# Optimization experiments

Hardware: AMD Instinct MI355X
Metric: run time of the kernel (lower is better)

The kernel has to match this reference:

```python
import jax, jax.numpy as jnp
import numpy as np

NUM_HEADS = 16
NUM_BUCKETS = 32
MAX_DISTANCE = 128


def _rel_bucket(rel):
    # bidirectional T5-style relative position bucketing
    nb = NUM_BUCKETS // 2
    ret = (rel > 0).astype(jnp.int32) * nb
    n = jnp.abs(rel)
    max_exact = nb // 2
    is_small = n < max_exact
    safe = jnp.maximum(n, 1).astype(jnp.float32)
    large = max_exact + (jnp.log(safe / max_exact) / np.log(MAX_DISTANCE / max_exact) * (nb - max_exact)).astype(jnp.int32)
    large = jnp.minimum(large, nb - 1)
    return ret + jnp.where(is_small, n, large)


def setup_inputs() -> dict:
    key = jax.random.key(0)
    ks = jax.random.split(key, 12)
    S, B, E = 1024, 4, 1024
    D = E // NUM_HEADS
    s = 0.02
    return {
        "query": jax.random.normal(ks[0], (S, B, E), jnp.float32),
        "q_w": jax.random.normal(ks[1], (E, E), jnp.float32) * s,
        "q_b": jnp.zeros((E,), jnp.float32),
        "k_w": jax.random.normal(ks[2], (E, E), jnp.float32) * s,
        "k_b": jnp.zeros((E,), jnp.float32),
        "v_w": jax.random.normal(ks[3], (E, E), jnp.float32) * s,
        "v_b": jnp.zeros((E,), jnp.float32),
        "out_w": jax.random.normal(ks[4], (E, E), jnp.float32) * s,
        "out_b": jnp.zeros((E,), jnp.float32),
        "rel_emb": jax.random.normal(ks[5], (NUM_BUCKETS, NUM_HEADS), jnp.float32) * s,
        "grep_w": jax.random.normal(ks[6], (8, D), jnp.float32) * s,
        "grep_b": jnp.zeros((8,), jnp.float32),
        "grep_a": jnp.ones((NUM_HEADS,), jnp.float32),
    }


def reference(query, q_w, q_b, k_w, k_b, v_w, v_b, out_w, out_b, rel_emb, grep_w, grep_b, grep_a):
    S, B, E = query.shape
    H = NUM_HEADS
    D = E // H
    scaling = D ** -0.5

    q = (query @ q_w.T + q_b) * scaling  # scaling applied before gating, as in WavLM
    k = query @ k_w.T + k_b
    v = query @ v_w.T + v_b

    def split(x):  # (S,B,E) -> (B,H,S,D)
        return x.reshape(S, B, H, D).transpose(1, 2, 0, 3)

    q4, k4, v4 = split(q), split(k), split(v)

    attn = jnp.einsum('bhqd,bhkd->bhqk', q4, k4)  # (B,H,S,S)

    pos = jnp.arange(S)
    bucket = _rel_bucket(pos[None, :] - pos[:, None])  # (S,S)
    pbias = rel_emb[bucket].transpose(2, 0, 1)          # (H,S,S)

    # GRU-gated relative position scaling
    g = jnp.einsum('bhsd,ed->bhse', q4, grep_w) + grep_b      # (B,H,S,8)
    g = jax.nn.sigmoid(g.reshape(B, H, S, 2, 4).sum(-1))     # (B,H,S,2)
    gate_a, gate_b = g[..., 0], g[..., 1]
    gate = gate_a * (gate_b * grep_a[None, :, None] - 1.0) + 2.0  # (B,H,S)

    attn = attn + gate[..., None] * pbias[None]
    probs = jax.nn.softmax(attn, axis=-1)
    ctx = jnp.einsum('bhqk,bhkd->bhqd', probs, v4)  # (B,H,S,D)
    out = ctx.transpose(2, 0, 1, 3).reshape(S, B, E) @ out_w.T + out_b
    return out
```

## Files before the change

### kernel.cpp

```cpp
#include <hip/hip_runtime.h>
#include <stdint.h>


typedef short bf16x8 __attribute__((ext_vector_type(8)));
typedef float f32x4 __attribute__((ext_vector_type(4)));

#define MFMA_BF16(a, b, c) __builtin_amdgcn_mfma_f32_16x16x32_bf16((a), (b), (c), 0, 0, 0)

#define LOG2E 1.44269504088896f
#define LN2 0.693147180559945f

__device__ __forceinline__ unsigned short f2bf(float x) {
  union { float f; unsigned u; } v; v.f = x;
  unsigned r = v.u + 0x7fffu + ((v.u >> 16) & 1u);
  return (unsigned short)(r >> 16);
}
__device__ __forceinline__ float bf2f(unsigned short u) {
  union { unsigned u; float f; } v; v.u = ((unsigned)u) << 16;
  return v.f;
}

__device__ __forceinline__ void gload_lds16(const void* g, void* l) {
  __builtin_amdgcn_global_load_lds(
      (const __attribute__((address_space(1))) unsigned int*)g,
      (__attribute__((address_space(3))) unsigned int*)l, 16, 0, 0);
}

__device__ __forceinline__ int swz(int row) { return (row ^ (row >> 2)) & 3; }

__global__ __launch_bounds__(256) void prep_kernel(
    const float* __restrict__ query, const float* __restrict__ q_w,
    const float* __restrict__ k_w, const float* __restrict__ v_w,
    const float* __restrict__ out_w, unsigned short* __restrict__ q_bf,
    unsigned short* __restrict__ wq, unsigned short* __restrict__ wk,
    unsigned short* __restrict__ wv, unsigned short* __restrict__ ohi,
    unsigned short* __restrict__ olo) {
  int i = blockIdx.x * 256 + threadIdx.x;
  if (i < 4194304) {
    int e = i & 1023;
    int sb = i >> 10;
    int s = sb >> 2, b = sb & 3;
    q_bf[((size_t)(b * 1024 + s) << 10) | e] = f2bf(query[i]);
  } else {
    int j = i - 4194304;
    wq[j] = f2bf(q_w[j]);
    wk[j] = f2bf(k_w[j]);
    wv[j] = f2bf(v_w[j]);
    float x = out_w[j];
    unsigned short h = f2bf(x);
    ohi[j] = h;
    olo[j] = f2bf(x - bf2f(h));
  }
}

__global__ __launch_bounds__(256) void relbias_kernel(const float* __restrict__ rel_emb,
                                                      float* __restrict__ bias_d) {
  int idx = blockIdx.x * 256 + threadIdx.x;
  if (idx >= 2048) return;
  if (idx == 2047) {
#pragma unroll
    for (int h = 0; h < 16; ++h) bias_d[h * 2048 + idx] = 0.f;
    return;
  }
  int rel = idx - 1023;
  int n = rel < 0 ? -rel : rel;
  int ret = rel > 0 ? 16 : 0;
  int bucket;
  if (n < 8) {
    bucket = ret + n;
  } else {
    int large = 8 + (int)(logf((float)n / 8.0f) / logf(16.0f) * 8.0f);
    if (large > 15) large = 15;
    bucket = ret + large;
  }
#pragma unroll
  for (int h = 0; h < 16; ++h)
    bias_d[h * 2048 + idx] = rel_emb[bucket * 16 + h] * LOG2E;
}

__global__ __launch_bounds__(256, 2) void qkv_gemm_kernel(
    const unsigned short* __restrict__ A, const unsigned short* __restrict__ Wq,
    const unsigned short* __restrict__ Wk, const unsigned short* __restrict__ Wv,
    const float* __restrict__ qb, const float* __restrict__ kb, const float* __restrict__ vb,
    unsigned short* __restrict__ qh,
    unsigned short* __restrict__ kh,
    unsigned short* __restrict__ vT)
{
  __shared__ __align__(16) unsigned short As[128 * 32];
  __shared__ __align__(16) unsigned short Bs[128 * 32];
  const int tid = threadIdx.x, lane = tid & 63;
  const int wv_ = tid >> 6;
  const int nt = blockIdx.x;
  const int mt = blockIdx.y;
  const int mat = nt >> 3;
  const unsigned short* W = mat == 0 ? Wq : (mat == 1 ? Wk : Wv);
  const int n0 = (nt & 7) * 128;
  const int m0 = mt * 128;
  const int moff = (wv_ & 1) * 64;
  const int noff = (wv_ >> 1) * 64;

  f32x4 acc[4][4] = {};
  const char* Ab = (const char*)A;
  const char* Wb = (const char*)W;

  int st_row[2], st_g[2];
#pragma unroll
  for (int c = 0; c < 2; ++c) {
    int o = c * 4096 + tid * 16;
    int row = o >> 6, p = (o >> 4) & 3;
    st_row[c] = row;
    st_g[c] = p ^ swz(row);
  }

  for (int kt = 0; kt < 32; ++kt) {
    __syncthreads();
#pragma unroll
    for (int c = 0; c < 2; ++c) {
      int o = c * 4096 + tid * 16;
      size_t ga = (size_t)(m0 + st_row[c]) * 2048 + (size_t)kt * 64 + st_g[c] * 16;
      size_t gb = (size_t)(n0 + st_row[c]) * 2048 + (size_t)kt * 64 + st_g[c] * 16;
      gload_lds16(Ab + ga, (char*)As + o);
      gload_lds16(Wb + gb, (char*)Bs + o);
    }
    __syncthreads();

    bf16x8 af[4], bfr[4];
#pragma unroll
    for (int i = 0; i < 4; ++i) {
      int ra = moff + i * 16 + (lane & 15);
      int rb = noff + i * 16 + (lane & 15);
      int q = lane >> 4;
      af[i] = *(const bf16x8*)((const char*)As + ra * 64 + (q ^ swz(ra)) * 16);
      bfr[i] = *(const bf16x8*)((const char*)Bs + rb * 64 + (q ^ swz(rb)) * 16);
    }
#pragma unroll
    for (int i = 0; i < 4; ++i)
#pragma unroll
      for (int j = 0; j < 4; ++j) acc[i][j] = MFMA_BF16(af[i], bfr[j], acc[i][j]);
  }

  const int bidx = m0 >> 10;
  const int s00 = (m0 & 1023) + moff + ((lane >> 4) << 2);
  const int c0 = n0 + noff + (lane & 15);
  if (mat < 2) {
    const float* barr = mat == 0 ? qb : kb;
    unsigned short* dst = mat == 0 ? qh : kh;
    const float scale = mat == 0 ? (0.125f * LOG2E) : 1.0f;
#pragma unroll
    for (int j = 0; j < 4; ++j) {
      int col = c0 + j * 16;
      int hh = col >> 6, dd = col & 63;
      float bias = barr[col];
#pragma unroll
      for (int i = 0; i < 4; ++i)
#pragma unroll
        for (int r = 0; r < 4; ++r) {
          int s = s00 + i * 16 + r;
          dst[((size_t)(bidx * 16 + hh) * 1024 + s) * 64 + dd] =
              f2bf((acc[i][j][r] + bias) * scale);
        }
    }
  } else {
#pragma unroll
    for (int j = 0; j < 4; ++j) {
      int col = c0 + j * 16;
      int hh = col >> 6, dd = col & 63;
      float bias = vb[col];
#pragma unroll
      for (int i = 0; i < 4; ++i) {
        int s = s00 + i * 16;
        ushort4 pk;
        pk.x = f2bf(acc[i][j][0] + bias);
        pk.y = f2bf(acc[i][j][1] + bias);
        pk.z = f2bf(acc[i][j][2] + bias);
        pk.w = f2bf(acc[i][j][3] + bias);
        *(ushort4*)&vT[((size_t)(bidx * 16 + hh) * 64 + dd) * 1024 + s] = pk;
      }
    }
  }
}

__global__ __launch_bounds__(256) void gate_kernel(const unsigned short* __restrict__ qh,
                                                   const float* __restrict__ grep_w,
                                                   const float* __restrict__ grep_b,
                                                   const float* __restrict__ grep_a,
                                                   float* __restrict__ gate) {
  __shared__ float gw[512];
  __shared__ float gbb[8];
  __shared__ float gaa[16];
  int tid = threadIdx.x;
  for (int i = tid; i < 512; i += 256) gw[i] = grep_w[i];
  if (tid < 8) gbb[tid] = grep_b[tid];
  if (tid < 16) gaa[tid] = grep_a[tid];
  __syncthreads();
  int idx = blockIdx.x * 256 + tid;
  int h = (idx >> 10) & 15;
  const unsigned short* qrow = qh + (size_t)idx * 64;
  float a[8] = {0.f, 0.f, 0.f, 0.f, 0.f, 0.f, 0.f, 0.f};
#pragma unroll
  for (int c = 0; c < 8; ++c) {
    bf16x8 v = *(const bf16x8*)(qrow + c * 8);
#pragma unroll
    for (int jj = 0; jj < 8; ++jj) {
      float qv = bf2f((unsigned short)v[jj]);
      int d = c * 8 + jj;
#pragma unroll
      for (int e = 0; e < 8; ++e) a[e] += qv * gw[e * 64 + d];
    }
  }
  float sa = (a[0] + a[1] + a[2] + a[3]) * LN2 + gbb[0] + gbb[1] + gbb[2] + gbb[3];
  float sb = (a[4] + a[5] + a[6] + a[7]) * LN2 + gbb[4] + gbb[5] + gbb[6] + gbb[7];
  float siga = 1.f / (1.f + __expf(-sa));
  float sigb = 1.f / (1.f + __expf(-sb));
  gate[idx] = siga * (sigb * gaa[h] - 1.f) + 2.f;
}

__global__ __launch_bounds__(512, 4) void attn_kernel(
    const unsigned short* __restrict__ qh, const unsigned short* __restrict__ kh,
    const unsigned short* __restrict__ vT, const float* __restrict__ gate,
    const float* __restrict__ bias_d, unsigned short* __restrict__ ctx_hi,
    unsigned short* __restrict__ ctx_lo) {
  __shared__ __align__(16) char smem[59392];
  const int tid = threadIdx.x, lane = tid & 63, w = tid >> 6;
  const int bh = blockIdx.x;
  const int h = bh & 15;
  const int s0 = blockIdx.y * 128;
  const int sqb = s0 + w * 16;
  const int q15 = lane & 15, quad = lane >> 4;

  float* biasrow = (float*)(smem + 51200);
  unsigned short* pw = (unsigned short*)(smem + 32768) + w * 1152 + q15 * 72;

  ((float4*)biasrow)[tid] = ((const float4*)(bias_d + h * 2048))[tid];

  const char* kbase = (const char*)(kh + (size_t)bh * 65536);
  const char* vbase = (const char*)(vT + (size_t)bh * 65536);

  const int o = tid * 16;
  const int srow = o >> 7;
  const int sg = ((o >> 4) & 7) ^ (srow & 7);
  const size_t koff = (size_t)srow * 128 + sg * 16;
  const size_t voff = (size_t)srow * 2048 + sg * 16;

  gload_lds16(kbase + koff, smem + o);
  gload_lds16(vbase + voff, smem + 16384 + o);

  const unsigned short* qbase = qh + ((size_t)bh * 1024 + sqb + q15) * 64 + (quad << 3);
  bf16x8 qf0 = *(const bf16x8*)(qbase);
  bf16x8 qf1 = *(const bf16x8*)(qbase + 32);

  const int sq = sqb + q15;
  const float gate_lane = gate[bh * 1024 + sq];

  float l_run = 0.f;
  f32x4 acc_o[4] = {};

  for (int kc = 0; kc < 16; ++kc) {
    __syncthreads();
    const char* Kc = smem + (kc & 1) * 8192;
    const char* Vc = smem + 16384 + (kc & 1) * 8192;
    if (kc < 15) {
      int nb = (kc + 1) & 1;
      gload_lds16(kbase + (size_t)(kc + 1) * 8192 + koff, smem + nb * 8192 + o);
      gload_lds16(vbase + (size_t)(kc + 1) * 128 + voff, smem + 16384 + nb * 8192 + o);
    }

    f32x4 sacc[4] = {};
#pragma unroll
    for (int t = 0; t < 4; ++t) {
      int key = t * 16 + q15;
#pragma unroll
      for (int dc = 0; dc < 2; ++dc) {
        int c16 = dc * 4 + quad;
        bf16x8 ak = *(const bf16x8*)(Kc + key * 128 + ((c16 ^ (key & 7)) << 4));
        sacc[t] = MFMA_BF16(ak, dc ? qf1 : qf0, sacc[t]);
      }
    }

    const int boff = kc * 64 - sq + 1023 + (quad << 2);
    float p[16];
    float ps = 0.f;
#pragma unroll
    for (int t = 0; t < 4; ++t)
#pragma unroll
      for (int r = 0; r < 4; ++r) {
        float v = __builtin_fmaf(gate_lane, biasrow[boff + t * 16 + r], sacc[t][r]);
        float e = __builtin_exp2f(v);
        p[t * 4 + r] = e;
        ps += e;
      }
    l_run += ps;

#pragma unroll
    for (int t = 0; t < 4; ++t) {
      ushort4 pk;
      pk.x = f2bf(p[t * 4 + 0]);
      pk.y = f2bf(p[t * 4 + 1]);
      pk.z = f2bf(p[t * 4 + 2]);
      pk.w = f2bf(p[t * 4 + 3]);
      *(ushort4*)(pw + t * 16 + (quad << 2)) = pk;
    }

#pragma unroll
    for (int ch = 0; ch < 2; ++ch) {
      bf16x8 pb = *(const bf16x8*)(pw + ch * 32 + (quad << 3));
#pragma unroll
      for (int t = 0; t < 4; ++t) {
        int d = t * 16 + q15;
        int c16 = ch * 4 + quad;
        bf16x8 av = *(const bf16x8*)(Vc + d * 128 + ((c16 ^ (d & 7)) << 4));
        acc_o[t] = MFMA_BF16(av, pb, acc_o[t]);
      }
    }
  }

  l_run += __shfl_xor(l_run, 16, 64);
  l_run += __shfl_xor(l_run, 32, 64);
  const float inv = 1.0f / l_run;

  __syncthreads();
  float* Ot = (float*)smem;
  {
    float* ow = Ot + (w * 16 + q15) * 65;
#pragma unroll
    for (int t = 0; t < 4; ++t)
#pragma unroll
      for (int r = 0; r < 4; ++r) ow[t * 16 + (quad << 2) + r] = acc_o[t][r] * inv;
  }
  __syncthreads();
  {
    int row = tid >> 2, dg = tid & 3;
    int s = s0 + row;
    const float* src = Ot + row * 65 + dg * 16;
    unsigned short hibuf[16], lobuf[16];
#pragma unroll
    for (int j = 0; j < 16; ++j) {
      float v = src[j];
      unsigned short hu = f2bf(v);
      hibuf[j] = hu;
      lobuf[j] = f2bf(v - bf2f(hu));
    }
    size_t base = (size_t)(s * 4 + (bh >> 4)) * 1024 + h * 64 + dg * 16;
#pragma unroll
    for (int half = 0; half < 2; ++half) {
      *(uint4*)(ctx_hi + base + half * 8) = *(const uint4*)(hibuf + half * 8);
      *(uint4*)(ctx_lo + base + half * 8) = *(const uint4*)(lobuf + half * 8);
    }
  }
}

__global__ __launch_bounds__(256, 3) void outproj_kernel(
    const unsigned short* __restrict__ Ahi, const unsigned short* __restrict__ Alo,
    const unsigned short* __restrict__ Bhi, const unsigned short* __restrict__ Blo,
    const float* __restrict__ ob, float* __restrict__ out) {
  __shared__ __align__(16) char smem[49152];
  const int tid = threadIdx.x, lane = tid & 63, wv_ = tid >> 6;
  const int q15 = lane & 15, quad = lane >> 4;
  const int n0 = blockIdx.x * 128;
  const int m0 = blockIdx.y * 64;
  const int moff = (wv_ & 1) * 32;
  const int noff = (wv_ >> 1) * 64;

  const int oa = tid * 16;
  const int ra_ = oa >> 6;
  const int ga_ = (((oa >> 4) & 3) ^ swz(ra_)) << 4;
  int rb_[2], gb_[2], obo_[2];
#pragma unroll
  for (int c = 0; c < 2; ++c) {
    int ob2 = c * 4096 + tid * 16;
    obo_[c] = ob2;
    rb_[c] = ob2 >> 6;
    gb_[c] = (((ob2 >> 4) & 3) ^ swz(rb_[c])) << 4;
  }

#define OP_STAGE(kt, buf)                                                        \
  {                                                                              \
    char* bb = smem + (buf)*24576;                                               \
    size_t ga = (size_t)(m0 + ra_) * 2048 + (size_t)(kt)*64 + ga_;               \
    gload_lds16((const char*)Ahi + ga, bb + oa);                                 \
    gload_lds16((const char*)Alo + ga, bb + 4096 + oa);                          \
    _Pragma("unroll") for (int c = 0; c < 2; ++c) {                              \
      size_t gb = (size_t)(n0 + rb_[c]) * 2048 + (size_t)(kt)*64 + gb_[c];       \
      gload_lds16((const char*)Bhi + gb, bb + 8192 + obo_[c]);                   \
      gload_lds16((const char*)Blo + gb, bb + 16384 + obo_[c]);                  \
    }                                                                            \
  }

  f32x4 acc[2][4] = {};
  OP_STAGE(0, 0);
  for (int kt = 0; kt < 32; ++kt) {
    __syncthreads();
    const char* base = smem + (kt & 1) * 24576;
    if (kt < 31) OP_STAGE(kt + 1, (kt + 1) & 1);

    bf16x8 ah[2], al[2], bhf[4], blf[4];
#pragma unroll
    for (int i = 0; i < 2; ++i) {
      int ra = moff + i * 16 + q15;
      int pa = (quad ^ swz(ra)) << 4;
      ah[i] = *(const bf16x8*)(base + ra * 64 + pa);
      al[i] = *(const bf16x8*)(base + 4096 + ra * 64 + pa);
    }
#pragma unroll
    for (int j = 0; j < 4; ++j) {
      int rb = noff + j * 16 + q15;
      int pb = (quad ^ swz(rb)) << 4;
      bhf[j] = *(const bf16x8*)(base + 8192 + rb * 64 + pb);
      blf[j] = *(const bf16x8*)(base + 16384 + rb * 64 + pb);
    }
#pragma unroll
    for (int i = 0; i < 2; ++i)
#pragma unroll
      for (int j = 0; j < 4; ++j) {
        f32x4 t = MFMA_BF16(al[i], bhf[j], acc[i][j]);
        t = MFMA_BF16(ah[i], blf[j], t);
        acc[i][j] = MFMA_BF16(ah[i], bhf[j], t);
      }
  }
#undef OP_STAGE

  const int rr0 = m0 + moff + (quad << 2);
  const int c0 = n0 + noff + q15;
#pragma unroll
  for (int j = 0; j < 4; ++j) {
    int col = c0 + j * 16;
    float bias = ob[col];
#pragma unroll
    for (int i = 0; i < 2; ++i)
#pragma unroll
      for (int r = 0; r < 4; ++r)
        out[(size_t)(rr0 + i * 16 + r) * 1024 + col] = acc[i][j][r] + bias;
  }
}

extern "C" void kernel_launch(void* const* d_in, const int* in_sizes, int n_in,
                              void* d_out, int out_size, void* d_ws, size_t ws_size,
                              hipStream_t stream) {
  const float* query = (const float*)d_in[0];
  const float* q_w = (const float*)d_in[1];
  const float* q_b = (const float*)d_in[2];
  const float* k_w = (const float*)d_in[3];
  const float* k_b = (const float*)d_in[4];
  const float* v_w = (const float*)d_in[5];
  const float* v_b = (const float*)d_in[6];
  const float* out_w = (const float*)d_in[7];
  const float* out_b = (const float*)d_in[8];
  const float* rel_emb = (const float*)d_in[9];
  const float* grep_w = (const float*)d_in[10];
  const float* grep_b = (const float*)d_in[11];
  const float* grep_a = (const float*)d_in[12];
  float* out = (float*)d_out;

  const size_t MB = 1u << 20;
  char* ws = (char*)d_ws;
  unsigned short* q_bf = (unsigned short*)(ws);
  unsigned short* wq_bf = (unsigned short*)(ws + 8 * MB);
  unsigned short* wk_bf = (unsigned short*)(ws + 10 * MB);
  unsigned short* wv_bf = (unsigned short*)(ws + 12 * MB);
  unsigned short* ow_hi = (unsigned short*)(ws + 14 * MB);
  unsigned short* ow_lo = (unsigned short*)(ws + 16 * MB);
  unsigned short* qhp = (unsigned short*)(ws + 18 * MB);
  unsigned short* khp = (unsigned short*)(ws + 26 * MB);
  unsigned short* vTp = (unsigned short*)(ws + 34 * MB);
  unsigned short* ctxh = (unsigned short*)(ws + 42 * MB);
  unsigned short* ctxl = (unsigned short*)(ws + 50 * MB);
  float* gatep = (float*)(ws + 58 * MB);
  float* biasp = (float*)(ws + 58 * MB + 256 * 1024);

  prep_kernel<<<20480, 256, 0, stream>>>(query, q_w, k_w, v_w, out_w, q_bf, wq_bf, wk_bf,
                                         wv_bf, ow_hi, ow_lo);
  relbias_kernel<<<8, 256, 0, stream>>>(rel_emb, biasp);
  qkv_gemm_kernel<<<dim3(24, 32), 256, 0, stream>>>(q_bf, wq_bf, wk_bf, wv_bf, q_b, k_b, v_b,
                                                    qhp, khp, vTp);
  gate_kernel<<<256, 256, 0, stream>>>(qhp, grep_w, grep_b, grep_a, gatep);
  attn_kernel<<<dim3(64, 8), 512, 0, stream>>>(qhp, khp, vTp, gatep, biasp, ctxh, ctxl);
  outproj_kernel<<<dim3(8, 64), 256, 0, stream>>>(ctxh, ctxl, ow_hi, ow_lo, out_b, out);
}
```

Measured before the change: 218.6 us.

## Double-buffer QKV GEMM, merge relbias into prep, shrink attention LDS

Folds the relative-bias table kernel into the prep kernel, removing one launch. Double-buffers the QKV GEMM's shared-memory tiles so the next K-slice load overlaps the MFMAs, dropping one barrier per iteration, and raises its occupancy hint. In attention, only the needed bias window is loaded, the per-warp P scratch is made compact with an XOR swizzle, and exp/pack is fused per tile, cutting LDS so more blocks fit per CU. The GEMM now uses 32KB of LDS per block, and the higher occupancy hints may cost registers or cause spills.

```diff
diff --git a/kernel.cpp b/kernel.cpp
--- a/kernel.cpp
+++ b/kernel.cpp
@@ -31,17 +31,18 @@
 __global__ __launch_bounds__(256) void prep_kernel(
     const float* __restrict__ query, const float* __restrict__ q_w,
     const float* __restrict__ k_w, const float* __restrict__ v_w,
-    const float* __restrict__ out_w, unsigned short* __restrict__ q_bf,
-    unsigned short* __restrict__ wq, unsigned short* __restrict__ wk,
-    unsigned short* __restrict__ wv, unsigned short* __restrict__ ohi,
-    unsigned short* __restrict__ olo) {
+    const float* __restrict__ out_w, const float* __restrict__ rel_emb,
+    unsigned short* __restrict__ q_bf, unsigned short* __restrict__ wq,
+    unsigned short* __restrict__ wk, unsigned short* __restrict__ wv,
+    unsigned short* __restrict__ ohi, unsigned short* __restrict__ olo,
+    float* __restrict__ bias_d) {
   int i = blockIdx.x * 256 + threadIdx.x;
   if (i < 4194304) {
     int e = i & 1023;
     int sb = i >> 10;
     int s = sb >> 2, b = sb & 3;
     q_bf[((size_t)(b * 1024 + s) << 10) | e] = f2bf(query[i]);
-  } else {
+  } else if (i < 5242880) {
     int j = i - 4194304;
     wq[j] = f2bf(q_w[j]);
     wk[j] = f2bf(k_w[j]);
@@ -50,35 +51,32 @@
     unsigned short h = f2bf(x);
     ohi[j] = h;
     olo[j] = f2bf(x - bf2f(h));
-  }
-}
-
-__global__ __launch_bounds__(256) void relbias_kernel(const float* __restrict__ rel_emb,
-                                                      float* __restrict__ bias_d) {
-  int idx = blockIdx.x * 256 + threadIdx.x;
-  if (idx >= 2048) return;
-  if (idx == 2047) {
-#pragma unroll
-    for (int h = 0; h < 16; ++h) bias_d[h * 2048 + idx] = 0.f;
-    return;
-  }
-  int rel = idx - 1023;
-  int n = rel < 0 ? -rel : rel;
-  int ret = rel > 0 ? 16 : 0;
-  int bucket;
-  if (n < 8) {
-    bucket = ret + n;
   } else {
-    int large = 8 + (int)(logf((float)n / 8.0f) / logf(16.0f) * 8.0f);
-    if (large > 15) large = 15;
-    bucket = ret + large;
-  }
-#pragma unroll
-  for (int h = 0; h < 16; ++h)
-    bias_d[h * 2048 + idx] = rel_emb[bucket * 16 + h] * LOG2E;
-}
-
-__global__ __launch_bounds__(256, 2) void qkv_gemm_kernel(
+    int idx = i - 5242880;
+    if (idx >= 2048) return;
+    if (idx == 2047) {
+#pragma unroll
+      for (int h = 0; h < 16; ++h) bias_d[h * 2048 + idx] = 0.f;
+      return;
+    }
+    int rel = idx - 1023;
+    int n = rel < 0 ? -rel : rel;
+    int ret = rel > 0 ? 16 : 0;
+    int bucket;
+    if (n < 8) {
+      bucket = ret + n;
+    } else {
+      int large = 8 + (int)(logf((float)n / 8.0f) / logf(16.0f) * 8.0f);
+      if (large > 15) large = 15;
+      bucket = ret + large;
+    }
+#pragma unroll
+    for (int h = 0; h < 16; ++h)
+      bias_d[h * 2048 + idx] = rel_emb[bucket * 16 + h] * LOG2E;
+  }
+}
+
+__global__ __launch_bounds__(256, 3) void qkv_gemm_kernel(
     const unsigned short* __restrict__ A, const unsigned short* __restrict__ Wq,
     const unsigned short* __restrict__ Wk, const unsigned short* __restrict__ Wv,
     const float* __restrict__ qb, const float* __restrict__ kb, const float* __restrict__ vb,
@@ -86,8 +84,7 @@
     unsigned short* __restrict__ kh,
     unsigned short* __restrict__ vT)
 {
-  __shared__ __align__(16) unsigned short As[128 * 32];
-  __shared__ __align__(16) unsigned short Bs[128 * 32];
+  __shared__ __align__(16) char smem[32768];
   const int tid = threadIdx.x, lane = tid & 63;
   const int wv_ = tid >> 6;
   const int nt = blockIdx.x;
@@ -112,17 +109,23 @@
     st_g[c] = p ^ swz(row);
   }
 
+#define QKV_STAGE(kt, buf)                                                     \
+  {                                                                            \
+    char* bb = smem + (buf)*16384;                                             \
+    _Pragma("unroll") for (int c = 0; c < 2; ++c) {                            \
+      int o = c * 4096 + tid * 16;                                             \
+      size_t ga = (size_t)(m0 + st_row[c]) * 2048 + (size_t)(kt)*64 + st_g[c] * 16; \
+      size_t gb = (size_t)(n0 + st_row[c]) * 2048 + (size_t)(kt)*64 + st_g[c] * 16; \
+      gload_lds16(Ab + ga, bb + o);                                            \
+      gload_lds16(Wb + gb, bb + 8192 + o);                                     \
+    }                                                                          \
+  }
+
+  QKV_STAGE(0, 0);
   for (int kt = 0; kt < 32; ++kt) {
     __syncthreads();
-#pragma unroll
-    for (int c = 0; c < 2; ++c) {
-      int o = c * 4096 + tid * 16;
-      size_t ga = (size_t)(m0 + st_row[c]) * 2048 + (size_t)kt * 64 + st_g[c] * 16;
-      size_t gb = (size_t)(n0 + st_row[c]) * 2048 + (size_t)kt * 64 + st_g[c] * 16;
-      gload_lds16(Ab + ga, (char*)As + o);
-      gload_lds16(Wb + gb, (char*)Bs + o);
-    }
-    __syncthreads();
+    const char* base = smem + (kt & 1) * 16384;
+    if (kt < 31) QKV_STAGE(kt + 1, (kt + 1) & 1);
 
     bf16x8 af[4], bfr[4];
 #pragma unroll
@@ -130,14 +133,15 @@
       int ra = moff + i * 16 + (lane & 15);
       int rb = noff + i * 16 + (lane & 15);
       int q = lane >> 4;
-      af[i] = *(const bf16x8*)((const char*)As + ra * 64 + (q ^ swz(ra)) * 16);
-      bfr[i] = *(const bf16x8*)((const char*)Bs + rb * 64 + (q ^ swz(rb)) * 16);
+      af[i] = *(const bf16x8*)(base + ra * 64 + (q ^ swz(ra)) * 16);
+      bfr[i] = *(const bf16x8*)(base + 8192 + rb * 64 + (q ^ swz(rb)) * 16);
     }
 #pragma unroll
     for (int i = 0; i < 4; ++i)
 #pragma unroll
       for (int j = 0; j < 4; ++j) acc[i][j] = MFMA_BF16(af[i], bfr[j], acc[i][j]);
   }
+#undef QKV_STAGE
 
   const int bidx = m0 >> 10;
   const int s00 = (m0 & 1023) + moff + ((lane >> 4) << 2);
@@ -215,23 +219,22 @@
   gate[idx] = siga * (sigb * gaa[h] - 1.f) + 2.f;
 }
 
-__global__ __launch_bounds__(512, 4) void attn_kernel(
+__global__ __launch_bounds__(512, 6) void attn_kernel(
     const unsigned short* __restrict__ qh, const unsigned short* __restrict__ kh,
     const unsigned short* __restrict__ vT, const float* __restrict__ gate,
     const float* __restrict__ bias_d, unsigned short* __restrict__ ctx_hi,
     unsigned short* __restrict__ ctx_lo) {
-  __shared__ __align__(16) char smem[59392];
+  __shared__ __align__(16) char smem[53760];
   const int tid = threadIdx.x, lane = tid & 63, w = tid >> 6;
   const int bh = blockIdx.x;
   const int h = bh & 15;
   const int s0 = blockIdx.y * 128;
   const int sqb = s0 + w * 16;
-  const int q15 = lane & 15, quad = lane >> 4;
-
-  float* biasrow = (float*)(smem + 51200);
-  unsigned short* pw = (unsigned short*)(smem + 32768) + w * 1152 + q15 * 72;
-
-  ((float4*)biasrow)[tid] = ((const float4*)(bias_d + h * 2048))[tid];
+  const int q15 = lane & 15, quad = lane >> 4, q7 = lane & 7;
+
+  float* biasw = (float*)(smem + 49152);
+  if (tid < 288)
+    ((float4*)biasw)[tid] = ((const float4*)(bias_d + h * 2048 + (896 - s0)))[tid];
 
   const char* kbase = (const char*)(kh + (size_t)bh * 65536);
   const char* vbase = (const char*)(vT + (size_t)bh * 65536);
@@ -251,6 +254,8 @@
 
   const int sq = sqb + q15;
   const float gate_lane = gate[bh * 1024 + sq];
+
+  unsigned short* psrow = (unsigned short*)(smem + 32768 + w * 2048) + q15 * 64;
 
   float l_run = 0.f;
   f32x4 acc_o[4] = {};
@@ -265,45 +270,35 @@
       gload_lds16(vbase + (size_t)(kc + 1) * 128 + voff, smem + 16384 + nb * 8192 + o);
     }
 
-    f32x4 sacc[4] = {};
+    const int boff = kc * 64 - sq + s0 + 127 + (quad << 2);
+    float ps = 0.f;
 #pragma unroll
     for (int t = 0; t < 4; ++t) {
+      f32x4 sacc = {};
       int key = t * 16 + q15;
 #pragma unroll
       for (int dc = 0; dc < 2; ++dc) {
         int c16 = dc * 4 + quad;
         bf16x8 ak = *(const bf16x8*)(Kc + key * 128 + ((c16 ^ (key & 7)) << 4));
-        sacc[t] = MFMA_BF16(ak, dc ? qf1 : qf0, sacc[t]);
+        sacc = MFMA_BF16(ak, dc ? qf1 : qf0, sacc);
       }
-    }
-
-    const int boff = kc * 64 - sq + 1023 + (quad << 2);
-    float p[16];
-    float ps = 0.f;
-#pragma unroll
-    for (int t = 0; t < 4; ++t)
-#pragma unroll
-      for (int r = 0; r < 4; ++r) {
-        float v = __builtin_fmaf(gate_lane, biasrow[boff + t * 16 + r], sacc[t][r]);
-        float e = __builtin_exp2f(v);
-        p[t * 4 + r] = e;
-        ps += e;
-      }
+      float p0 = __builtin_exp2f(__builtin_fmaf(gate_lane, biasw[boff + t * 16 + 0], sacc[0]));
+      float p1 = __builtin_exp2f(__builtin_fmaf(gate_lane, biasw[boff + t * 16 + 1], sacc[1]));
+      float p2 = __builtin_exp2f(__builtin_fmaf(gate_lane, biasw[boff + t * 16 + 2], sacc[2]));
+      float p3 = __builtin_exp2f(__builtin_fmaf(gate_lane, biasw[boff + t * 16 + 3], sacc[3]));
+      ps += (p0 + p1) + (p2 + p3);
+      ushort4 pk;
+      pk.x = f2bf(p0); pk.y = f2bf(p1); pk.z = f2bf(p2); pk.w = f2bf(p3);
+      int c = t * 4 + quad;
+      int pc = (c >> 1) ^ q7;
+      *(ushort4*)(psrow + pc * 8 + (c & 1) * 4) = pk;
+    }
     l_run += ps;
 
 #pragma unroll
-    for (int t = 0; t < 4; ++t) {
-      ushort4 pk;
-      pk.x = f2bf(p[t * 4 + 0]);
-      pk.y = f2bf(p[t * 4 + 1]);
-      pk.z = f2bf(p[t * 4 + 2]);
-      pk.w = f2bf(p[t * 4 + 3]);
-      *(ushort4*)(pw + t * 16 + (quad << 2)) = pk;
-    }
-
-#pragma unroll
     for (int ch = 0; ch < 2; ++ch) {
-      bf16x8 pb = *(const bf16x8*)(pw + ch * 32 + (quad << 3));
+      int j = (ch * 4 + quad) ^ q7;
+      bf16x8 pb = *(const bf16x8*)(psrow + j * 8);
 #pragma unroll
       for (int t = 0; t < 4; ++t) {
         int d = t * 16 + q15;
@@ -467,9 +462,8 @@
   float* gatep = (float*)(ws + 58 * MB);
   float* biasp = (float*)(ws + 58 * MB + 256 * 1024);
 
-  prep_kernel<<<20480, 256, 0, stream>>>(query, q_w, k_w, v_w, out_w, q_bf, wq_bf, wk_bf,
-                                         wv_bf, ow_hi, ow_lo);
-  relbias_kernel<<<8, 256, 0, stream>>>(rel_emb, biasp);
+  prep_kernel<<<20488, 256, 0, stream>>>(query, q_w, k_w, v_w, out_w, rel_emb, q_bf, wq_bf,
+                                         wk_bf, wv_bf, ow_hi, ow_lo, biasp);
   qkv_gemm_kernel<<<dim3(24, 32), 256, 0, stream>>>(q_bf, wq_bf, wk_bf, wv_bf, q_b, k_b, v_b,
                                                     qhp, khp, vTp);
   gate_kernel<<<256, 256, 0, stream>>>(qhp, grep_w, grep_b, grep_a, gatep);
```

Result: faster. 211.4 us (-3.3%).
